# Optimization experiments

Measured on AMD Instinct MI355X. Metric: run time of the kernel, lower is better.

## Reference

```python
import jax, jax.numpy as jnp
import numpy as np

MAX_LENGTH = 10
SOS = 0
H = 1024
V = 32000
B = 256
S = 64


def setup_inputs() -> dict:
    key = jax.random.key(0)
    ks = jax.random.split(key, 16)
    sc = 1.0 / np.sqrt(H)
    return {
        "encoder_outputs": jax.random.normal(ks[0], (B, S, H), jnp.float32),
        "encoder_hidden": jax.random.normal(ks[1], (1, B, H), jnp.float32),
        "target_tensor": jax.random.randint(ks[2], (B, MAX_LENGTH), 0, V),
        "embedding": jax.random.normal(ks[3], (V, H), jnp.float32),
        "Wa_w": jax.random.uniform(ks[4], (H, H), jnp.float32, -sc, sc),
        "Wa_b": jax.random.uniform(ks[5], (H,), jnp.float32, -sc, sc),
        "Ua_w": jax.random.uniform(ks[6], (H, H), jnp.float32, -sc, sc),
        "Ua_b": jax.random.uniform(ks[7], (H,), jnp.float32, -sc, sc),
        "Va_w": jax.random.uniform(ks[8], (1, H), jnp.float32, -sc, sc),
        "Va_b": jax.random.uniform(ks[9], (1,), jnp.float32, -sc, sc),
        "gru_w_ih": jax.random.uniform(ks[10], (3 * H, 2 * H), jnp.float32, -sc, sc),
        "gru_w_hh": jax.random.uniform(ks[11], (3 * H, H), jnp.float32, -sc, sc),
        "gru_b_ih": jax.random.uniform(ks[12], (3 * H,), jnp.float32, -sc, sc),
        "gru_b_hh": jax.random.uniform(ks[13], (3 * H,), jnp.float32, -sc, sc),
        "out_w": jax.random.uniform(ks[14], (V, H), jnp.float32, -sc, sc),
        "out_b": jax.random.uniform(ks[15], (V,), jnp.float32, -sc, sc),
    }


def reference(encoder_outputs, encoder_hidden, target_tensor, embedding,
              Wa_w, Wa_b, Ua_w, Ua_b, Va_w, Va_b,
              gru_w_ih, gru_w_hh, gru_b_ih, gru_b_hh, out_w, out_b):
    keys = encoder_outputs                      # [B,S,H]
    # Ua(keys) is step-invariant: hoist out of the decode loop.
    Uk = jnp.einsum('bsh,kh->bsk', keys, Ua_w) + Ua_b  # [B,S,H]
    h0 = encoder_hidden[0]                      # [B,H]
    # teacher forcing: input at step i is SOS for i=0 else target[:, i-1]
    toks = jnp.concatenate(
        [jnp.full((B, 1), SOS, dtype=target_tensor.dtype),
         target_tensor[:, :MAX_LENGTH - 1]], axis=1).T  # [T,B]

    def step(h, tok):
        emb = embedding[tok]                               # [B,H] (dropout = identity in eval)
        wq = jnp.dot(h, Wa_w.T) + Wa_b                     # [B,H]
        e = jnp.tanh(wq[:, None, :] + Uk)                  # [B,S,H]
        scores = jnp.einsum('bsh,h->bs', e, Va_w[0]) + Va_b[0]
        w = jax.nn.softmax(scores, axis=-1)                # [B,S]
        ctx = jnp.einsum('bs,bsh->bh', w, keys)            # [B,H]
        x = jnp.concatenate([emb, ctx], axis=-1)           # [B,2H]
        gi = jnp.dot(x, gru_w_ih.T) + gru_b_ih             # [B,3H]
        gh = jnp.dot(h, gru_w_hh.T) + gru_b_hh             # [B,3H]
        ir, iz, inn = jnp.split(gi, 3, axis=-1)
        hr, hz, hn = jnp.split(gh, 3, axis=-1)
        r = jax.nn.sigmoid(ir + hr)
        z = jax.nn.sigmoid(iz + hz)
        n = jnp.tanh(inn + r * hn)
        h2 = (1.0 - z) * n + z * h                         # [B,H]
        logits = jnp.dot(h2, out_w.T) + out_b              # [B,V]
        return h2, (logits, w)

    h_last, (logits, attn) = jax.lax.scan(step, h0, toks)
    dec_out = jax.nn.log_softmax(jnp.transpose(logits, (1, 0, 2)), axis=-1)  # [B,T,V]
    attentions = jnp.transpose(attn, (1, 0, 2))            # [B,T,S]
    return dec_out, h_last[None, :, :], attentions
```

## Files before the change

### kernel.cpp

```cpp
#include <hip/hip_runtime.h>
#include <math.h>

#define H 1024
#define V 32000
#define B 256
#define S 64
#define T 10

#define GBK 32

typedef __attribute__((ext_vector_type(8))) short bf16x8;
typedef __attribute__((ext_vector_type(4))) float f32x4;

static __device__ __forceinline__ unsigned short f2bf(float f) {
  unsigned int u = __float_as_uint(f);
  u += 0x7fff + ((u >> 16) & 1);
  return (unsigned short)(u >> 16);
}
static __device__ __forceinline__ float bf2f(unsigned short u) {
  return __uint_as_float(((unsigned int)u) << 16);
}
static __device__ __forceinline__ float fast_tanh(float x) {
  float e = __expf(2.f * x);
  return 1.f - 2.f * __builtin_amdgcn_rcpf(e + 1.f);
}
static __device__ __forceinline__ float fast_sigmoid(float x) {
  return __builtin_amdgcn_rcpf(1.f + __expf(-x));
}

static __device__ __forceinline__ void load_lds16(const void* g, void* l) {
  __builtin_amdgcn_global_load_lds(
      (const __attribute__((address_space(1))) unsigned int*)g,
      (__attribute__((address_space(3))) unsigned int*)l, 16, 0, 0);
}

static __device__ __forceinline__ int lds_off(int row, int g) {
  return row * GBK + ((g ^ ((row >> 1) & 3)) * 8);
}

template <int TM, int TN, int MODE, int GRIDMODE, int STAGES>
__global__ __launch_bounds__(256) void gemm_mfma(
    const unsigned short* __restrict__ A, const unsigned short* __restrict__ W,
    const float* __restrict__ aux, float* __restrict__ C,
    unsigned short* __restrict__ Cb,
    int M, int N, int K, int ldc) {
  constexpr int FM = TM / 32;
  constexpr int FN = TN / 32;
  constexpr int CA = TM / 64;
  constexpr int CB = TN / 64;
  constexpr int LOADS = CA + CB;
  constexpr int F = (STAGES >= 3) ? (STAGES - 2) : 0;

  __shared__ unsigned short lsA[STAGES][TM * GBK];
  __shared__ unsigned short lsB[STAGES][TN * GBK];
  const int tid = threadIdx.x;
  const int lane = tid & 63;
  const int w = tid >> 6;

  int mIdx, nIdx;
  if constexpr (GRIDMODE == 1) {
    const int nwg = gridDim.x * gridDim.y;
    const int orig = blockIdx.y * gridDim.x + blockIdx.x;
    const int q = nwg >> 3, rr = nwg & 7;
    const int xcd = orig & 7, rest = orig >> 3;
    const int wgid =
        (xcd < rr ? xcd * (q + 1) : rr * (q + 1) + (xcd - rr) * q) + rest;
    mIdx = wgid % gridDim.x;
    nIdx = wgid / gridDim.x;
  } else {
    mIdx = blockIdx.y;
    nIdx = blockIdx.x;
  }
  const int mBase = mIdx * TM;
  const int nBase = nIdx * TN;
  const int rowBase = (w >> 1) * (TM / 2);
  const int colBase = (w & 1) * (TN / 2);

  const int fr = lane & 15;
  const int fkU = lane >> 4;
  const int fg = lane >> 4;

  f32x4 acc[FM][FN] = {};

  auto STAGE = [&](int buf, int k0) {
#pragma unroll
    for (int i = 0; i < CA; ++i) {
      int chunk = i * 256 + tid;
      int row = chunk >> 2;
      int u = chunk & 3;
      int col = (u ^ ((row >> 1) & 3)) * 8;
      load_lds16(A + (size_t)(mBase + row) * K + k0 + col,
                 &lsA[buf][chunk * 8]);
    }
#pragma unroll
    for (int i = 0; i < CB; ++i) {
      int chunk = i * 256 + tid;
      int row = chunk >> 2;
      int u = chunk & 3;
      int col = (u ^ ((row >> 1) & 3)) * 8;
      load_lds16(W + (size_t)(nBase + row) * K + k0 + col,
                 &lsB[buf][chunk * 8]);
    }
  };

  const int NT = K / GBK;
  for (int s = 0; s <= F && s < NT; ++s) STAGE(s % STAGES, s * GBK);

  for (int t = 0; t < NT; ++t) {
    const int rem = NT - 1 - t;
    if (rem >= F) {
      asm volatile("s_waitcnt vmcnt(%0)\n\ts_barrier" :: "i"(F * LOADS)
                   : "memory");
    } else if (rem == 2) {
      asm volatile("s_waitcnt vmcnt(%0)\n\ts_barrier" :: "i"(2 * LOADS)
                   : "memory");
    } else if (rem == 1) {
      asm volatile("s_waitcnt vmcnt(%0)\n\ts_barrier" :: "i"(1 * LOADS)
                   : "memory");
    } else {
      asm volatile("s_waitcnt vmcnt(0)\n\ts_barrier" ::: "memory");
    }
    if (t + F + 1 < NT) STAGE((t + F + 1) % STAGES, (t + F + 1) * GBK);

    const int cb = t % STAGES;
    bf16x8 af[FM], bfr[FN];
#pragma unroll
    for (int m = 0; m < FM; ++m)
      af[m] = *(const bf16x8*)&lsA[cb][lds_off(rowBase + m * 16 + fr, fkU)];
#pragma unroll
    for (int n = 0; n < FN; ++n)
      bfr[n] = *(const bf16x8*)&lsB[cb][lds_off(colBase + n * 16 + fr, fkU)];
#pragma unroll
    for (int m = 0; m < FM; ++m)
#pragma unroll
      for (int n = 0; n < FN; ++n)
        acc[m][n] = __builtin_amdgcn_mfma_f32_16x16x32_bf16(
            af[m], bfr[n], acc[m][n], 0, 0, 0);
  }

#pragma unroll
  for (int m = 0; m < FM; ++m) {
    int colg[FN];
    float bv[FN];
#pragma unroll
    for (int n = 0; n < FN; ++n) {
      colg[n] = nBase + colBase + n * 16 + fr;
      if constexpr (MODE != 2) bv[n] = aux[colg[n]];
    }
#pragma unroll
    for (int r = 0; r < 4; ++r) {
      const int rowg = mBase + rowBase + m * 16 + fg * 4 + r;
      float v[FN];
#pragma unroll
      for (int n = 0; n < FN; ++n) {
        if constexpr (MODE == 2)
          v[n] = acc[m][n][r] + aux[(size_t)rowg * ldc + colg[n]];
        else
          v[n] = acc[m][n][r] + bv[n];
        if constexpr (MODE == 1)
          Cb[(size_t)rowg * ldc + colg[n]] = f2bf(v[n]);
        else
          C[(size_t)rowg * ldc + colg[n]] = v[n];
      }
    }
  }
}

__global__ __launch_bounds__(256) void gemm_gru3(
    const unsigned short* __restrict__ A,
    const unsigned short* __restrict__ W3,
    const float* __restrict__ giE_t,
    const float* __restrict__ wqgh,
    const float* __restrict__ h_in,
    float* __restrict__ h_out,
    unsigned short* __restrict__ h_out_bf,
    unsigned char* __restrict__ h_out_f8) {
  constexpr int BK = 64;
  constexpr int STAGES = 3;
  constexpr int LOADS = 5;
  __shared__ unsigned short lsA[STAGES][64 * BK];
  __shared__ unsigned short lsW[STAGES][96 * BK];
  const int tid = threadIdx.x;
  const int lane = tid & 63;
  const int w = tid >> 6;
  const int mBase = blockIdx.x * 64;
  const int jBase = blockIdx.y * 32;
  const int fr = lane & 15;
  const int fkU = lane >> 4;
  const int fg = lane >> 4;

  f32x4 acc[6] = {};

  auto STAGE = [&](int buf, int k0) {
#pragma unroll
    for (int i = 0; i < 2; ++i) {
      int c = i * 256 + tid;
      int row = c >> 3, u = c & 7;
      int col = (u ^ (row & 7)) * 8;
      load_lds16(A + (size_t)(mBase + row) * H + k0 + col, &lsA[buf][c * 8]);
    }
#pragma unroll
    for (int i = 0; i < 3; ++i) {
      int c = i * 256 + tid;
      int wr = c >> 3, u = c & 7;
      int gate = wr >> 5, jj = wr & 31;
      int col = (u ^ (wr & 7)) * 8;
      load_lds16(W3 + (size_t)(gate * H + jBase + jj) * H + k0 + col,
                 &lsW[buf][c * 8]);
    }
  };

  const int NT = H / BK;
  STAGE(0, 0);
  STAGE(1, BK);
  for (int t = 0; t < NT; ++t) {
    const int rem = NT - 1 - t;
    if (rem >= 1) {
      asm volatile("s_waitcnt vmcnt(%0)\n\ts_barrier" :: "i"(LOADS)
                   : "memory");
    } else {
      asm volatile("s_waitcnt vmcnt(0)\n\ts_barrier" ::: "memory");
    }
    if (t + 2 < NT) STAGE((t + 2) % STAGES, (t + 2) * BK);
    const int cb = t % STAGES;
    const int arow = w * 16 + fr;
#pragma unroll
    for (int ks = 0; ks < 2; ++ks) {
      const int u = ks * 4 + fkU;
      bf16x8 af =
          *(const bf16x8*)&lsA[cb][arow * BK + ((u ^ (arow & 7)) * 8)];
#pragma unroll
      for (int n = 0; n < 6; ++n) {
        int wr = n * 16 + fr;
        bf16x8 bf =
            *(const bf16x8*)&lsW[cb][wr * BK + ((u ^ (wr & 7)) * 8)];
        acc[n] = __builtin_amdgcn_mfma_f32_16x16x32_bf16(af, bf, acc[n],
                                                         0, 0, 0);
      }
    }
  }

#pragma unroll
  for (int r = 0; r < 4; ++r) {
    const int b = mBase + w * 16 + fg * 4 + r;
    const float* giE_row = giE_t + (size_t)b * 3 * H;
    const float* gh_row = wqgh + (size_t)b * 4 * H + H;
#pragma unroll
    for (int jjg = 0; jjg < 2; ++jjg) {
      const int col = jBase + jjg * 16 + fr;
      float gr = acc[0 + jjg][r] + giE_row[col];
      float gz = acc[2 + jjg][r] + giE_row[H + col];
      float gn = acc[4 + jjg][r] + giE_row[2 * H + col];
      float rr = fast_sigmoid(gr + gh_row[col]);
      float zz = fast_sigmoid(gz + gh_row[H + col]);
      float nn = fast_tanh(gn + rr * gh_row[2 * H + col]);
      float hp = h_in[(size_t)b * H + col];
      float ho = (1.f - zz) * nn + zz * hp;
      h_out[(size_t)b * H + col] = ho;
      h_out_bf[(size_t)b * H + col] = f2bf(ho);
      int p8 = __builtin_amdgcn_cvt_pk_fp8_f32(ho, ho, 0, false);
      h_out_f8[(size_t)b * H + col] = (unsigned char)(p8 & 0xff);
    }
  }
}

__global__ __launch_bounds__(256) void gemm_fp8_logits(
    const unsigned char* __restrict__ A8, const unsigned char* __restrict__ W8,
    const float* __restrict__ bias, unsigned short* __restrict__ Cb,
    float* __restrict__ partials, int M, int N, int K, int ldc, int pstride) {
  constexpr int BK = 64;
  __shared__ __align__(16) unsigned char lsA[2][128 * BK];
  __shared__ __align__(16) unsigned char lsB[2][128 * BK];
  const int tid = threadIdx.x;
  const int lane = tid & 63;
  const int w = tid >> 6;

  const int nwg = gridDim.x * gridDim.y;
  const int orig = blockIdx.y * gridDim.x + blockIdx.x;
  const int q = nwg >> 3, rr = nwg & 7;
  const int xcd = orig & 7, rest = orig >> 3;
  const int wgid =
      (xcd < rr ? xcd * (q + 1) : rr * (q + 1) + (xcd - rr) * q) + rest;
  const int mIdx = wgid % gridDim.x;
  const int nIdx = wgid / gridDim.x;
  const int mBase = mIdx * 128;
  const int nBase = nIdx * 128;
  const int rowBase = (w >> 1) * 64;
  const int colBase = (w & 1) * 64;
  const int fr = lane & 15;
  const int fkU = lane >> 4;
  const int fg = lane >> 4;

  f32x4 acc[4][4] = {};

  auto STAGE = [&](int buf, int k0) {
#pragma unroll
    for (int i = 0; i < 2; ++i) {
      int c = i * 256 + tid;
      int row = c >> 2;
      int u = c & 3;
      int col = (u ^ ((row >> 1) & 3)) * 16;
      load_lds16(A8 + (size_t)(mBase + row) * K + k0 + col, &lsA[buf][c * 16]);
    }
#pragma unroll
    for (int i = 0; i < 2; ++i) {
      int c = i * 256 + tid;
      int row = c >> 2;
      int u = c & 3;
      int col = (u ^ ((row >> 1) & 3)) * 16;
      load_lds16(W8 + (size_t)(nBase + row) * K + k0 + col, &lsB[buf][c * 16]);
    }
  };

  const int NT = K / BK;
  STAGE(0, 0);
  int cb = 0;
  for (int t = 0; t < NT; ++t) {
    asm volatile("s_waitcnt vmcnt(0)\n\ts_barrier" ::: "memory");
    if (t + 1 < NT) STAGE(cb ^ 1, (t + 1) * BK);
#pragma unroll
    for (int ks = 0; ks < 2; ++ks) {
      const int u = ks * 2 + (fkU >> 1);
      const int sub = (fkU & 1) * 8;
      long long af[4], bf[4];
#pragma unroll
      for (int m = 0; m < 4; ++m) {
        int row = rowBase + m * 16 + fr;
        af[m] = *(const long long*)
            &lsA[cb][row * BK + ((u ^ ((row >> 1) & 3)) << 4) + sub];
      }
#pragma unroll
      for (int n = 0; n < 4; ++n) {
        int row = colBase + n * 16 + fr;
        bf[n] = *(const long long*)
            &lsB[cb][row * BK + ((u ^ ((row >> 1) & 3)) << 4) + sub];
      }
#pragma unroll
      for (int m = 0; m < 4; ++m)
#pragma unroll
        for (int n = 0; n < 4; ++n)
          acc[m][n] = __builtin_amdgcn_mfma_f32_16x16x32_fp8_fp8(
              af[m], bf[n], acc[m][n], 0, 0, 0);
    }
    cb ^= 1;
  }

#pragma unroll
  for (int m = 0; m < 4; ++m) {
    int colg[4];
    float bv[4];
#pragma unroll
    for (int n = 0; n < 4; ++n) {
      colg[n] = nBase + colBase + n * 16 + fr;
      bv[n] = bias[colg[n]];
    }
#pragma unroll
    for (int r = 0; r < 4; ++r) {
      const int rowg = mBase + rowBase + m * 16 + fg * 4 + r;
      float v[4];
#pragma unroll
      for (int n = 0; n < 4; ++n) {
        v[n] = acc[m][n][r] + bv[n];
        Cb[(size_t)rowg * ldc + colg[n]] = f2bf(v[n]);
      }
      float mx = fmaxf(fmaxf(v[0], v[1]), fmaxf(v[2], v[3]));
      mx = fmaxf(mx, __shfl_xor(mx, 1, 64));
      mx = fmaxf(mx, __shfl_xor(mx, 2, 64));
      mx = fmaxf(mx, __shfl_xor(mx, 4, 64));
      mx = fmaxf(mx, __shfl_xor(mx, 8, 64));
      float se = __expf(v[0] - mx) + __expf(v[1] - mx) +
                 __expf(v[2] - mx) + __expf(v[3] - mx);
      se += __shfl_xor(se, 1, 64);
      se += __shfl_xor(se, 2, 64);
      se += __shfl_xor(se, 4, 64);
      se += __shfl_xor(se, 8, 64);
      if (fr == 0) {
        float2* pp = (float2*)partials;
        pp[(size_t)rowg * pstride + nIdx * 2 + (w & 1)] = make_float2(mx, se);
      }
    }
  }
}

__global__ __launch_bounds__(256) void cvt_bf16_kernel(
    const float* __restrict__ src, unsigned short* __restrict__ dst) {
  size_t i = ((size_t)blockIdx.x * 256 + threadIdx.x) * 8;
  float4 a = *(const float4*)&src[i];
  float4 b = *(const float4*)&src[i + 4];
  ushort4 lo, hi;
  lo.x = f2bf(a.x); lo.y = f2bf(a.y); lo.z = f2bf(a.z); lo.w = f2bf(a.w);
  hi.x = f2bf(b.x); hi.y = f2bf(b.y); hi.z = f2bf(b.z); hi.w = f2bf(b.w);
  *(ushort4*)&dst[i] = lo;
  *(ushort4*)&dst[i + 4] = hi;
}

__global__ __launch_bounds__(256) void cvt_fp8_kernel(
    const float* __restrict__ src, unsigned int* __restrict__ dst) {
  size_t i = (size_t)blockIdx.x * 256 + threadIdx.x;
  float4 a = ((const float4*)src)[i * 2];
  float4 b = ((const float4*)src)[i * 2 + 1];
  int lo = __builtin_amdgcn_cvt_pk_fp8_f32(a.x, a.y, 0, false);
  lo = __builtin_amdgcn_cvt_pk_fp8_f32(a.z, a.w, lo, true);
  int hi = __builtin_amdgcn_cvt_pk_fp8_f32(b.x, b.y, 0, false);
  hi = __builtin_amdgcn_cvt_pk_fp8_f32(b.z, b.w, hi, true);
  ((int2*)dst)[i] = make_int2(lo, hi);
}

__global__ __launch_bounds__(256) void cvt_split_wih(
    const float* __restrict__ w_ih, unsigned short* __restrict__ Wemb,
    unsigned short* __restrict__ Wctx) {
  size_t base = ((size_t)blockIdx.x * 256 + threadIdx.x) * 8;
  int row = (int)(base >> 11);
  int col = (int)(base & 2047);
  float4 a = *(const float4*)&w_ih[base];
  float4 b = *(const float4*)&w_ih[base + 4];
  ushort4 lo, hi;
  lo.x = f2bf(a.x); lo.y = f2bf(a.y); lo.z = f2bf(a.z); lo.w = f2bf(a.w);
  hi.x = f2bf(b.x); hi.y = f2bf(b.y); hi.z = f2bf(b.z); hi.w = f2bf(b.w);
  unsigned short* dst = (col < H) ? (Wemb + (size_t)row * H + col)
                                  : (Wctx + (size_t)row * H + col - H);
  *(ushort4*)dst = lo;
  *(ushort4*)(dst + 4) = hi;
}

__global__ __launch_bounds__(256) void build_fused_bias(
    const float* __restrict__ Wa_b, const float* __restrict__ b_hh,
    float* __restrict__ fb) {
  int i = blockIdx.x * 256 + threadIdx.x;
  fb[i] = (i < H) ? Wa_b[i] : b_hh[i - H];
}

__global__ __launch_bounds__(256) void embed_all_kernel(
    const int* __restrict__ target, const float* __restrict__ emb,
    unsigned short* __restrict__ embAll) {
  int idx = blockIdx.x * 256 + threadIdx.x;
  int h8 = (idx & 127) * 8;
  int tb = idx >> 7;
  int t = tb >> 8;
  int b = tb & 255;
  int tok = (t == 0) ? 0 : target[b * T + (t - 1)];
  const float* e = emb + (size_t)tok * H + h8;
  float4 a = *(const float4*)e;
  float4 c = *(const float4*)(e + 4);
  ushort4 lo, hi;
  lo.x = f2bf(a.x); lo.y = f2bf(a.y); lo.z = f2bf(a.z); lo.w = f2bf(a.w);
  hi.x = f2bf(c.x); hi.y = f2bf(c.y); hi.z = f2bf(c.z); hi.w = f2bf(c.w);
  unsigned short* d = embAll + (size_t)tb * H + h8;
  *(ushort4*)d = lo;
  *(ushort4*)(d + 4) = hi;
}

__global__ __launch_bounds__(256) void attn_fused_kernel(
    const float* __restrict__ wqgh, const unsigned short* __restrict__ Uk_bf,
    const unsigned short* __restrict__ keys_bf,
    const float* __restrict__ Va_w, const float* __restrict__ Va_b,
    float* __restrict__ out_attn, unsigned short* __restrict__ ctx_bf, int t) {
  const int b = blockIdx.x;
  const int tid = threadIdx.x;
  __shared__ float wqs[H];
  __shared__ float vas[H];
  __shared__ float sw[S];

  ((float4*)wqs)[tid] = ((const float4*)(wqgh + (size_t)b * 4 * H))[tid];
  ((float4*)vas)[tid] = ((const float4*)Va_w)[tid];
  __syncthreads();

  const int s = tid >> 2;
  const int hc = (tid & 3) * 256;
  const unsigned short* uk = Uk_bf + ((size_t)b * S + s) * H + hc;
  float sum = 0.f;
#pragma unroll 4
  for (int i = 0; i < 256; i += 8) {
    bf16x8 u = *(const bf16x8*)&uk[i];
#pragma unroll
    for (int j = 0; j < 8; ++j) {
      float e = fast_tanh(wqs[hc + i + j] + bf2f((unsigned short)u[j]));
      sum += e * vas[hc + i + j];
    }
  }
  sum += __shfl_xor(sum, 1, 64);
  sum += __shfl_xor(sum, 2, 64);
  if ((tid & 3) == 0) sw[s] = sum + Va_b[0];
  __syncthreads();

  if (tid < 64) {
    float v = sw[tid];
    float m = v;
    for (int off = 32; off > 0; off >>= 1) m = fmaxf(m, __shfl_xor(m, off, 64));
    float e = __expf(v - m);
    float sm = e;
    for (int off = 32; off > 0; off >>= 1) sm += __shfl_xor(sm, off, 64);
    float wv = e / sm;
    sw[tid] = wv;
    out_attn[((size_t)b * T + t) * S + tid] = wv;
  }
  __syncthreads();

  const unsigned short* kb = keys_bf + (size_t)b * S * H + tid * 4;
  float c0 = 0.f, c1 = 0.f, c2 = 0.f, c3 = 0.f;
#pragma unroll 8
  for (int s2 = 0; s2 < S; ++s2) {
    float wv = sw[s2];
    ushort4 kv = *(const ushort4*)&kb[(size_t)s2 * H];
    c0 += wv * bf2f(kv.x);
    c1 += wv * bf2f(kv.y);
    c2 += wv * bf2f(kv.z);
    c3 += wv * bf2f(kv.w);
  }
  ushort4 o;
  o.x = f2bf(c0); o.y = f2bf(c1); o.z = f2bf(c2); o.w = f2bf(c3);
  *(ushort4*)&ctx_bf[(size_t)b * H + tid * 4] = o;
}

__global__ __launch_bounds__(256) void logsm_reduce_kernel(
    const float* __restrict__ partials, float* __restrict__ ls, int P) {
  const int row = blockIdx.x;
  const int tid = threadIdx.x;
  const float2* pp = (const float2*)partials + (size_t)row * P;
  __shared__ float red[256];
  float mx = -INFINITY;
  for (int i = tid; i < P; i += 256) mx = fmaxf(mx, pp[i].x);
  red[tid] = mx;
  __syncthreads();
  for (int off = 128; off > 0; off >>= 1) {
    if (tid < off) red[tid] = fmaxf(red[tid], red[tid + off]);
    __syncthreads();
  }
  mx = red[0];
  __syncthreads();
  float sm = 0.f;
  for (int i = tid; i < P; i += 256) sm += pp[i].y * __expf(pp[i].x - mx);
  red[tid] = sm;
  __syncthreads();
  for (int off = 128; off > 0; off >>= 1) {
    if (tid < off) red[tid] += red[tid + off];
    __syncthreads();
  }
  if (tid == 0) ls[row] = mx + __logf(red[0]);
}

__global__ __launch_bounds__(256) void logsm_sub_kernel(
    const unsigned short* __restrict__ logits_bf, const float* __restrict__ ls,
    float* __restrict__ dec) {
  const int tb = blockIdx.y;
  const int t = tb >> 8;
  const int b = tb & 255;
  const int i8 = (blockIdx.x * 256 + threadIdx.x) * 8;
  if (i8 < V) {
    float l = ls[tb];
    const unsigned short* src = logits_bf + (size_t)tb * V + i8;
    bf16x8 u = *(const bf16x8*)src;
    float* d = dec + (size_t)b * T * V + (size_t)t * V + i8;
    float4 o0, o1;
    o0.x = bf2f((unsigned short)u[0]) - l; o0.y = bf2f((unsigned short)u[1]) - l;
    o0.z = bf2f((unsigned short)u[2]) - l; o0.w = bf2f((unsigned short)u[3]) - l;
    o1.x = bf2f((unsigned short)u[4]) - l; o1.y = bf2f((unsigned short)u[5]) - l;
    o1.z = bf2f((unsigned short)u[6]) - l; o1.w = bf2f((unsigned short)u[7]) - l;
    *(float4*)d = o0;
    *(float4*)(d + 4) = o1;
  }
}

__global__ __launch_bounds__(256) void copy_kernel(
    const float* __restrict__ src, float* __restrict__ dst, int n) {
  int i = blockIdx.x * 256 + threadIdx.x;
  if (i < n) dst[i] = src[i];
}

extern "C" void kernel_launch(void* const* d_in, const int* in_sizes, int n_in,
                              void* d_out, int out_size, void* d_ws, size_t ws_size,
                              hipStream_t stream) {
  const float* keys       = (const float*)d_in[0];
  const float* enc_hidden = (const float*)d_in[1];
  const int*   target     = (const int*)d_in[2];
  const float* embedding  = (const float*)d_in[3];
  const float* Wa_w = (const float*)d_in[4];
  const float* Wa_b = (const float*)d_in[5];
  const float* Ua_w = (const float*)d_in[6];
  const float* Ua_b = (const float*)d_in[7];
  const float* Va_w = (const float*)d_in[8];
  const float* Va_b = (const float*)d_in[9];
  const float* gru_w_ih = (const float*)d_in[10];
  const float* gru_w_hh = (const float*)d_in[11];
  const float* gru_b_ih = (const float*)d_in[12];
  const float* gru_b_hh = (const float*)d_in[13];
  const float* out_w = (const float*)d_in[14];
  const float* out_b = (const float*)d_in[15];

  float* out = (float*)d_out;
  float* out_dec  = out;
  float* out_h    = out + (size_t)B * T * V;
  float* out_attn = out + (size_t)B * T * V + (size_t)B * H;

  char* p = (char*)d_ws;
  unsigned short* keys_bf = (unsigned short*)p; p += (size_t)B * S * H * 2;
  unsigned char*  outw8   = (unsigned char*)p;  p += (size_t)V * H;
  unsigned short* Uaw_bf  = (unsigned short*)p; p += (size_t)H * H * 2;
  unsigned short* fusedW  = (unsigned short*)p; p += (size_t)4 * H * H * 2;
  float*          fusedB  = (float*)p;          p += (size_t)4 * H * 4;
  unsigned short* Wemb_bf = (unsigned short*)p; p += (size_t)3 * H * H * 2;
  unsigned short* Wctx_bf = (unsigned short*)p; p += (size_t)3 * H * H * 2;
  unsigned short* embAll  = (unsigned short*)p; p += (size_t)T * B * H * 2;
  unsigned short* Uk_bf   = (unsigned short*)p; p += (size_t)B * S * H * 2;
  float*          giE     = (float*)p;          p += (size_t)T * B * 3 * H * 4;
  float*          wqgh    = (float*)p;          p += (size_t)B * 4 * H * 4;
  unsigned short* ctx_bf  = (unsigned short*)p; p += (size_t)B * H * 2;
  float*          hA      = (float*)p;          p += (size_t)B * H * 4;
  float*          hB      = (float*)p;          p += (size_t)B * H * 4;
  unsigned short* hAll    = (unsigned short*)p; p += (size_t)(T + 1) * B * H * 2;
  unsigned char*  hAll8   = (unsigned char*)p;  p += (size_t)T * B * H;
  unsigned short* logits_bf = (unsigned short*)p; p += (size_t)T * B * V * 2;
  float*          parts   = (float*)p;          p += (size_t)T * B * 500 * 2 * 4;
  float*          ls      = (float*)p;          p += (size_t)T * B * 4;

  cvt_bf16_kernel<<<(B * S * H) / 2048, 256, 0, stream>>>(keys, keys_bf);
  cvt_fp8_kernel<<<((size_t)V * H) / 2048, 256, 0, stream>>>(
      out_w, (unsigned int*)outw8);
  cvt_bf16_kernel<<<(H * H) / 2048, 256, 0, stream>>>(Ua_w, Uaw_bf);
  cvt_bf16_kernel<<<(H * H) / 2048, 256, 0, stream>>>(Wa_w, fusedW);
  cvt_bf16_kernel<<<(3 * H * H) / 2048, 256, 0, stream>>>(gru_w_hh,
                                                          fusedW + (size_t)H * H);
  build_fused_bias<<<(4 * H) / 256, 256, 0, stream>>>(Wa_b, gru_b_hh, fusedB);
  cvt_split_wih<<<(3 * H * 2 * H) / 2048, 256, 0, stream>>>(gru_w_ih, Wemb_bf,
                                                            Wctx_bf);
  embed_all_kernel<<<(T * B * H / 8) / 256, 256, 0, stream>>>(target, embedding,
                                                              embAll);
  cvt_bf16_kernel<<<(B * H) / 2048, 256, 0, stream>>>(enc_hidden, hAll);

  gemm_mfma<128, 128, 1, 0, 2>
      <<<dim3(H / 128, (B * S) / 128), 256, 0, stream>>>(
          keys_bf, Uaw_bf, Ua_b, nullptr, Uk_bf, B * S, H, H, H);
  gemm_mfma<128, 128, 0, 1, 2>
      <<<dim3((T * B) / 128, 3 * H / 128), 256, 0, stream>>>(
          embAll, Wemb_bf, gru_b_ih, giE, nullptr, T * B, 3 * H, H, 3 * H);

  const float* h_in = enc_hidden;
  float* hbufs[2] = {hA, hB};

  for (int t = 0; t < T; ++t) {
    const unsigned short* hbf_in = hAll + (size_t)t * B * H;
    unsigned short* hbf_out = hAll + (size_t)(t + 1) * B * H;
    unsigned char* h8_out = hAll8 + (size_t)t * B * H;
    float* h_out = hbufs[t & 1];

    gemm_mfma<64, 64, 0, 1, 5><<<dim3(B / 64, 4 * H / 64), 256, 0, stream>>>(
        hbf_in, fusedW, fusedB, wqgh, nullptr, B, 4 * H, H, 4 * H);
    attn_fused_kernel<<<B, 256, 0, stream>>>(
        wqgh, Uk_bf, keys_bf, Va_w, Va_b, out_attn, ctx_bf, t);
    gemm_gru3<<<dim3(B / 64, H / 32), 256, 0, stream>>>(
        ctx_bf, Wctx_bf, giE + (size_t)t * B * 3 * H, wqgh, h_in, h_out,
        hbf_out, h8_out);

    h_in = h_out;
  }

  gemm_fp8_logits<<<dim3((T * B) / 128, V / 128), 256, 0, stream>>>(
      hAll8, outw8, out_b, logits_bf, parts, T * B, V, H, V, 500);
  logsm_reduce_kernel<<<T * B, 256, 0, stream>>>(parts, ls, 500);
  logsm_sub_kernel<<<dim3((V + 2047) / 2048, T * B), 256, 0, stream>>>(
      logits_bf, ls, out_dec);

  copy_kernel<<<(B * H + 255) / 256, 256, 0, stream>>>(h_in, out_h, B * H);
}
```

Measured before the change: 941.5 us.

## Store keys, Ua weights and Uk in fp8; compute Uk with fp8 GEMM

Keys and Ua_w are converted to fp8 instead of bf16. The hoisted Uk projection now runs on the templated fp8 MFMA GEMM and writes fp8 output, and the per-step attention kernel reads fp8 Uk and keys, halving the bytes it streams on every decode step. Three weight-conversion launches are also merged into one prep_weights kernel to cut launch count. The cost is lower precision in the attention scores and context, which may push accuracy close to tolerance.

```diff
diff --git a/kernel.cpp b/kernel.cpp
--- a/kernel.cpp
+++ b/kernel.cpp
@@ -42,7 +42,6 @@
 __global__ __launch_bounds__(256) void gemm_mfma(
     const unsigned short* __restrict__ A, const unsigned short* __restrict__ W,
     const float* __restrict__ aux, float* __restrict__ C,
-    unsigned short* __restrict__ Cb,
     int M, int N, int K, int ldc) {
   constexpr int FM = TM / 32;
   constexpr int FN = TN / 32;
@@ -157,10 +156,7 @@
           v[n] = acc[m][n][r] + aux[(size_t)rowg * ldc + colg[n]];
         else
           v[n] = acc[m][n][r] + bv[n];
-        if constexpr (MODE == 1)
-          Cb[(size_t)rowg * ldc + colg[n]] = f2bf(v[n]);
-        else
-          C[(size_t)rowg * ldc + colg[n]] = v[n];
+        C[(size_t)rowg * ldc + colg[n]] = v[n];
       }
     }
   }
@@ -264,10 +260,12 @@
   }
 }
 
-__global__ __launch_bounds__(256) void gemm_fp8_logits(
+template <int MODE>
+__global__ __launch_bounds__(256) void gemm_fp8(
     const unsigned char* __restrict__ A8, const unsigned char* __restrict__ W8,
     const float* __restrict__ bias, unsigned short* __restrict__ Cb,
-    float* __restrict__ partials, int M, int N, int K, int ldc, int pstride) {
+    unsigned char* __restrict__ C8, float* __restrict__ partials,
+    int M, int N, int K, int ldc, int pstride) {
   constexpr int BK = 64;
   __shared__ __align__(16) unsigned char lsA[2][128 * BK];
   __shared__ __align__(16) unsigned char lsB[2][128 * BK];
@@ -361,30 +359,37 @@
 #pragma unroll
       for (int n = 0; n < 4; ++n) {
         v[n] = acc[m][n][r] + bv[n];
-        Cb[(size_t)rowg * ldc + colg[n]] = f2bf(v[n]);
+        if constexpr (MODE == 3) {
+          Cb[(size_t)rowg * ldc + colg[n]] = f2bf(v[n]);
+        } else {
+          int pk = __builtin_amdgcn_cvt_pk_fp8_f32(v[n], v[n], 0, false);
+          C8[(size_t)rowg * ldc + colg[n]] = (unsigned char)(pk & 0xff);
+        }
       }
-      float mx = fmaxf(fmaxf(v[0], v[1]), fmaxf(v[2], v[3]));
-      mx = fmaxf(mx, __shfl_xor(mx, 1, 64));
-      mx = fmaxf(mx, __shfl_xor(mx, 2, 64));
-      mx = fmaxf(mx, __shfl_xor(mx, 4, 64));
-      mx = fmaxf(mx, __shfl_xor(mx, 8, 64));
-      float se = __expf(v[0] - mx) + __expf(v[1] - mx) +
-                 __expf(v[2] - mx) + __expf(v[3] - mx);
-      se += __shfl_xor(se, 1, 64);
-      se += __shfl_xor(se, 2, 64);
-      se += __shfl_xor(se, 4, 64);
-      se += __shfl_xor(se, 8, 64);
-      if (fr == 0) {
-        float2* pp = (float2*)partials;
-        pp[(size_t)rowg * pstride + nIdx * 2 + (w & 1)] = make_float2(mx, se);
+      if constexpr (MODE == 3) {
+        float mx = fmaxf(fmaxf(v[0], v[1]), fmaxf(v[2], v[3]));
+        mx = fmaxf(mx, __shfl_xor(mx, 1, 64));
+        mx = fmaxf(mx, __shfl_xor(mx, 2, 64));
+        mx = fmaxf(mx, __shfl_xor(mx, 4, 64));
+        mx = fmaxf(mx, __shfl_xor(mx, 8, 64));
+        float se = __expf(v[0] - mx) + __expf(v[1] - mx) +
+                   __expf(v[2] - mx) + __expf(v[3] - mx);
+        se += __shfl_xor(se, 1, 64);
+        se += __shfl_xor(se, 2, 64);
+        se += __shfl_xor(se, 4, 64);
+        se += __shfl_xor(se, 8, 64);
+        if (fr == 0) {
+          float2* pp = (float2*)partials;
+          pp[(size_t)rowg * pstride + nIdx * 2 + (w & 1)] =
+              make_float2(mx, se);
+        }
       }
     }
   }
 }
 
-__global__ __launch_bounds__(256) void cvt_bf16_kernel(
-    const float* __restrict__ src, unsigned short* __restrict__ dst) {
-  size_t i = ((size_t)blockIdx.x * 256 + threadIdx.x) * 8;
+static __device__ __forceinline__ void cvt8(const float* src,
+                                            unsigned short* dst, size_t i) {
   float4 a = *(const float4*)&src[i];
   float4 b = *(const float4*)&src[i + 4];
   ushort4 lo, hi;
@@ -392,6 +397,37 @@
   hi.x = f2bf(b.x); hi.y = f2bf(b.y); hi.z = f2bf(b.z); hi.w = f2bf(b.w);
   *(ushort4*)&dst[i] = lo;
   *(ushort4*)&dst[i + 4] = hi;
+}
+
+__global__ __launch_bounds__(256) void cvt_bf16_kernel(
+    const float* __restrict__ src, unsigned short* __restrict__ dst) {
+  cvt8(src, dst, ((size_t)blockIdx.x * 256 + threadIdx.x) * 8);
+}
+
+__global__ __launch_bounds__(256) void prep_weights(
+    const float* __restrict__ Wa_w, const float* __restrict__ w_hh,
+    const float* __restrict__ w_ih, unsigned short* __restrict__ fusedW,
+    unsigned short* __restrict__ Wemb, unsigned short* __restrict__ Wctx) {
+  const int blk = blockIdx.x;
+  if (blk < 512) {
+    cvt8(Wa_w, fusedW, ((size_t)blk * 256 + threadIdx.x) * 8);
+  } else if (blk < 2048) {
+    cvt8(w_hh, fusedW + (size_t)H * H,
+         ((size_t)(blk - 512) * 256 + threadIdx.x) * 8);
+  } else {
+    size_t base = ((size_t)(blk - 2048) * 256 + threadIdx.x) * 8;
+    int row = (int)(base >> 11);
+    int col = (int)(base & 2047);
+    float4 a = *(const float4*)&w_ih[base];
+    float4 b = *(const float4*)&w_ih[base + 4];
+    ushort4 lo, hi;
+    lo.x = f2bf(a.x); lo.y = f2bf(a.y); lo.z = f2bf(a.z); lo.w = f2bf(a.w);
+    hi.x = f2bf(b.x); hi.y = f2bf(b.y); hi.z = f2bf(b.z); hi.w = f2bf(b.w);
+    unsigned short* dst = (col < H) ? (Wemb + (size_t)row * H + col)
+                                    : (Wctx + (size_t)row * H + col - H);
+    *(ushort4*)dst = lo;
+    *(ushort4*)(dst + 4) = hi;
+  }
 }
 
 __global__ __launch_bounds__(256) void cvt_fp8_kernel(
@@ -404,23 +440,6 @@
   int hi = __builtin_amdgcn_cvt_pk_fp8_f32(b.x, b.y, 0, false);
   hi = __builtin_amdgcn_cvt_pk_fp8_f32(b.z, b.w, hi, true);
   ((int2*)dst)[i] = make_int2(lo, hi);
-}
-
-__global__ __launch_bounds__(256) void cvt_split_wih(
-    const float* __restrict__ w_ih, unsigned short* __restrict__ Wemb,
-    unsigned short* __restrict__ Wctx) {
-  size_t base = ((size_t)blockIdx.x * 256 + threadIdx.x) * 8;
-  int row = (int)(base >> 11);
-  int col = (int)(base & 2047);
-  float4 a = *(const float4*)&w_ih[base];
-  float4 b = *(const float4*)&w_ih[base + 4];
-  ushort4 lo, hi;
-  lo.x = f2bf(a.x); lo.y = f2bf(a.y); lo.z = f2bf(a.z); lo.w = f2bf(a.w);
-  hi.x = f2bf(b.x); hi.y = f2bf(b.y); hi.z = f2bf(b.z); hi.w = f2bf(b.w);
-  unsigned short* dst = (col < H) ? (Wemb + (size_t)row * H + col)
-                                  : (Wctx + (size_t)row * H + col - H);
-  *(ushort4*)dst = lo;
-  *(ushort4*)(dst + 4) = hi;
 }
 
 __global__ __launch_bounds__(256) void build_fused_bias(
@@ -451,8 +470,8 @@
 }
 
 __global__ __launch_bounds__(256) void attn_fused_kernel(
-    const float* __restrict__ wqgh, const unsigned short* __restrict__ Uk_bf,
-    const unsigned short* __restrict__ keys_bf,
+    const float* __restrict__ wqgh, const unsigned char* __restrict__ Uk_f8,
+    const unsigned char* __restrict__ keys_f8,
     const float* __restrict__ Va_w, const float* __restrict__ Va_b,
     float* __restrict__ out_attn, unsigned short* __restrict__ ctx_bf, int t) {
   const int b = blockIdx.x;
@@ -467,14 +486,23 @@
 
   const int s = tid >> 2;
   const int hc = (tid & 3) * 256;
-  const unsigned short* uk = Uk_bf + ((size_t)b * S + s) * H + hc;
+  const unsigned char* uk = Uk_f8 + ((size_t)b * S + s) * H + hc;
   float sum = 0.f;
 #pragma unroll 4
   for (int i = 0; i < 256; i += 8) {
-    bf16x8 u = *(const bf16x8*)&uk[i];
+    uint2 u = *(const uint2*)&uk[i];
+    float uv[8];
+    uv[0] = __builtin_amdgcn_cvt_f32_fp8(u.x, 0);
+    uv[1] = __builtin_amdgcn_cvt_f32_fp8(u.x, 1);
+    uv[2] = __builtin_amdgcn_cvt_f32_fp8(u.x, 2);
+    uv[3] = __builtin_amdgcn_cvt_f32_fp8(u.x, 3);
+    uv[4] = __builtin_amdgcn_cvt_f32_fp8(u.y, 0);
+    uv[5] = __builtin_amdgcn_cvt_f32_fp8(u.y, 1);
+    uv[6] = __builtin_amdgcn_cvt_f32_fp8(u.y, 2);
+    uv[7] = __builtin_amdgcn_cvt_f32_fp8(u.y, 3);
 #pragma unroll
     for (int j = 0; j < 8; ++j) {
-      float e = fast_tanh(wqs[hc + i + j] + bf2f((unsigned short)u[j]));
+      float e = fast_tanh(wqs[hc + i + j] + uv[j]);
       sum += e * vas[hc + i + j];
     }
   }
@@ -496,16 +524,16 @@
   }
   __syncthreads();
 
-  const unsigned short* kb = keys_bf + (size_t)b * S * H + tid * 4;
+  const unsigned char* kb = keys_f8 + (size_t)b * S * H + tid * 4;
   float c0 = 0.f, c1 = 0.f, c2 = 0.f, c3 = 0.f;
 #pragma unroll 8
   for (int s2 = 0; s2 < S; ++s2) {
     float wv = sw[s2];
-    ushort4 kv = *(const ushort4*)&kb[(size_t)s2 * H];
-    c0 += wv * bf2f(kv.x);
-    c1 += wv * bf2f(kv.y);
-    c2 += wv * bf2f(kv.z);
-    c3 += wv * bf2f(kv.w);
+    unsigned int kv = *(const unsigned int*)&kb[(size_t)s2 * H];
+    c0 += wv * __builtin_amdgcn_cvt_f32_fp8(kv, 0);
+    c1 += wv * __builtin_amdgcn_cvt_f32_fp8(kv, 1);
+    c2 += wv * __builtin_amdgcn_cvt_f32_fp8(kv, 2);
+    c3 += wv * __builtin_amdgcn_cvt_f32_fp8(kv, 3);
   }
   ushort4 o;
   o.x = f2bf(c0); o.y = f2bf(c1); o.z = f2bf(c2); o.w = f2bf(c3);
@@ -593,15 +621,15 @@
   float* out_attn = out + (size_t)B * T * V + (size_t)B * H;
 
   char* p = (char*)d_ws;
-  unsigned short* keys_bf = (unsigned short*)p; p += (size_t)B * S * H * 2;
+  unsigned char*  keys_f8 = (unsigned char*)p;  p += (size_t)B * S * H;
   unsigned char*  outw8   = (unsigned char*)p;  p += (size_t)V * H;
-  unsigned short* Uaw_bf  = (unsigned short*)p; p += (size_t)H * H * 2;
+  unsigned char*  Uaw8    = (unsigned char*)p;  p += (size_t)H * H;
   unsigned short* fusedW  = (unsigned short*)p; p += (size_t)4 * H * H * 2;
   float*          fusedB  = (float*)p;          p += (size_t)4 * H * 4;
   unsigned short* Wemb_bf = (unsigned short*)p; p += (size_t)3 * H * H * 2;
   unsigned short* Wctx_bf = (unsigned short*)p; p += (size_t)3 * H * H * 2;
   unsigned short* embAll  = (unsigned short*)p; p += (size_t)T * B * H * 2;
-  unsigned short* Uk_bf   = (unsigned short*)p; p += (size_t)B * S * H * 2;
+  unsigned char*  Uk_f8   = (unsigned char*)p;  p += (size_t)B * S * H;
   float*          giE     = (float*)p;          p += (size_t)T * B * 3 * H * 4;
   float*          wqgh    = (float*)p;          p += (size_t)B * 4 * H * 4;
   unsigned short* ctx_bf  = (unsigned short*)p; p += (size_t)B * H * 2;
@@ -613,26 +641,24 @@
   float*          parts   = (float*)p;          p += (size_t)T * B * 500 * 2 * 4;
   float*          ls      = (float*)p;          p += (size_t)T * B * 4;
 
-  cvt_bf16_kernel<<<(B * S * H) / 2048, 256, 0, stream>>>(keys, keys_bf);
+  cvt_fp8_kernel<<<(B * S * H) / 2048, 256, 0, stream>>>(
+      keys, (unsigned int*)keys_f8);
   cvt_fp8_kernel<<<((size_t)V * H) / 2048, 256, 0, stream>>>(
       out_w, (unsigned int*)outw8);
-  cvt_bf16_kernel<<<(H * H) / 2048, 256, 0, stream>>>(Ua_w, Uaw_bf);
-  cvt_bf16_kernel<<<(H * H) / 2048, 256, 0, stream>>>(Wa_w, fusedW);
-  cvt_bf16_kernel<<<(3 * H * H) / 2048, 256, 0, stream>>>(gru_w_hh,
-                                                          fusedW + (size_t)H * H);
+  cvt_fp8_kernel<<<(H * H) / 2048, 256, 0, stream>>>(
+      Ua_w, (unsigned int*)Uaw8);
+  prep_weights<<<5120, 256, 0, stream>>>(Wa_w, gru_w_hh, gru_w_ih,
+                                         fusedW, Wemb_bf, Wctx_bf);
   build_fused_bias<<<(4 * H) / 256, 256, 0, stream>>>(Wa_b, gru_b_hh, fusedB);
-  cvt_split_wih<<<(3 * H * 2 * H) / 2048, 256, 0, stream>>>(gru_w_ih, Wemb_bf,
-                                                            Wctx_bf);
   embed_all_kernel<<<(T * B * H / 8) / 256, 256, 0, stream>>>(target, embedding,
                                                               embAll);
   cvt_bf16_kernel<<<(B * H) / 2048, 256, 0, stream>>>(enc_hidden, hAll);
 
-  gemm_mfma<128, 128, 1, 0, 2>
-      <<<dim3(H / 128, (B * S) / 128), 256, 0, stream>>>(
-          keys_bf, Uaw_bf, Ua_b, nullptr, Uk_bf, B * S, H, H, H);
+  gemm_fp8<4><<<dim3((B * S) / 128, H / 128), 256, 0, stream>>>(
+      keys_f8, Uaw8, Ua_b, nullptr, Uk_f8, nullptr, B * S, H, H, H, 0);
   gemm_mfma<128, 128, 0, 1, 2>
       <<<dim3((T * B) / 128, 3 * H / 128), 256, 0, stream>>>(
-          embAll, Wemb_bf, gru_b_ih, giE, nullptr, T * B, 3 * H, H, 3 * H);
+          embAll, Wemb_bf, gru_b_ih, giE, T * B, 3 * H, H, 3 * H);
 
   const float* h_in = enc_hidden;
   float* hbufs[2] = {hA, hB};
@@ -644,9 +670,9 @@
     float* h_out = hbufs[t & 1];
 
     gemm_mfma<64, 64, 0, 1, 5><<<dim3(B / 64, 4 * H / 64), 256, 0, stream>>>(
-        hbf_in, fusedW, fusedB, wqgh, nullptr, B, 4 * H, H, 4 * H);
+        hbf_in, fusedW, fusedB, wqgh, B, 4 * H, H, 4 * H);
     attn_fused_kernel<<<B, 256, 0, stream>>>(
-        wqgh, Uk_bf, keys_bf, Va_w, Va_b, out_attn, ctx_bf, t);
+        wqgh, Uk_f8, keys_f8, Va_w, Va_b, out_attn, ctx_bf, t);
     gemm_gru3<<<dim3(B / 64, H / 32), 256, 0, stream>>>(
         ctx_bf, Wctx_bf, giE + (size_t)t * B * 3 * H, wqgh, h_in, h_out,
         hbf_out, h8_out);
@@ -654,8 +680,8 @@
     h_in = h_out;
   }
 
-  gemm_fp8_logits<<<dim3((T * B) / 128, V / 128), 256, 0, stream>>>(
-      hAll8, outw8, out_b, logits_bf, parts, T * B, V, H, V, 500);
+  gemm_fp8<3><<<dim3((T * B) / 128, V / 128), 256, 0, stream>>>(
+      hAll8, outw8, out_b, logits_bf, nullptr, parts, T * B, V, H, V, 500);
   logsm_reduce_kernel<<<T * B, 256, 0, stream>>>(parts, ls, 500);
   logsm_sub_kernel<<<dim3((V + 2047) / 2048, T * B), 256, 0, stream>>>(
       logits_bf, ls, out_dec);
```

Measured after the change: 895.4 us. -4.9%, faster.
